# Kernel optimization log

Measured on AMD Instinct MI355X. Metric: run time of the kernel, lower is better.

## Reference

```python
import jax, jax.numpy as jnp
import numpy as np
import math

B, T = 512, 512
ENC = 512          # 2 * input_size
N_MELS, R = 80, 2
ATTN, DEC = 256, 256
PRE_H, PRE_O = 256, 256
HID = 128          # DCA hidden
SC, SK = 8, 21     # static channels / kernel
DC, DK = 8, 21     # dynamic channels / kernel
PL, PA, PB = 11, 0.1, 0.9  # prior length, alpha, beta


def _betabinom_pmf(k, n, a, b):
    lg = math.lgamma
    return math.exp(lg(n + 1) - lg(k + 1) - lg(n - k + 1)
                    + lg(k + a) + lg(n - k + b) - lg(n + a + b)
                    - (lg(a) + lg(b) - lg(a + b)))


def setup_inputs() -> dict:
    key = jax.random.key(0)
    ks = iter(jax.random.split(key, 64))
    def rn(shape, s=0.05):
        return jax.random.normal(next(ks), shape, dtype=jnp.float32) * s
    inp = {}
    inp["h"] = rn([B, T, ENC], 1.0)
    inp["y"] = rn([B, N_MELS], 1.0)
    a = jax.random.uniform(next(ks), [B, T], dtype=jnp.float32)
    inp["alpha"] = a / a.sum(-1, keepdims=True)  # valid attention distribution
    inp["c"] = rn([B, ENC], 1.0)
    for n in ["attn_h0", "attn_c0", "rnn1_h0", "rnn1_c0", "rnn2_h0", "rnn2_c0"]:
        inp[n] = rn([B, ATTN], 1.0)
    # prenet
    inp["fc1_w"] = rn([PRE_H, N_MELS]); inp["fc1_b"] = rn([PRE_H])
    inp["fc2_w"] = rn([PRE_O, PRE_H]); inp["fc2_b"] = rn([PRE_O])
    # dynamic convolution attention
    inp["W_w"] = rn([HID, ATTN]); inp["W_b"] = rn([HID])
    inp["V_w"] = rn([DC * DK, HID])
    inp["F_w"] = rn([SC, 1, SK])
    inp["U_w"] = rn([HID, SC])
    inp["T_w"] = rn([HID, DC]); inp["T_b"] = rn([HID])
    inp["v_w"] = rn([1, HID])
    P = np.array([_betabinom_pmf(k, PL - 1, PA, PB) for k in range(PL)], np.float32)[::-1].copy()
    inp["P"] = jnp.asarray(P)
    # attn LSTM cell: input = 2*input_size + prenet output = 768
    inp["attn_wih"] = rn([4 * ATTN, ENC + PRE_O]); inp["attn_whh"] = rn([4 * ATTN, ATTN])
    inp["attn_bih"] = rn([4 * ATTN]); inp["attn_bhh"] = rn([4 * ATTN])
    inp["lin_w"] = rn([DEC, ENC + ATTN]); inp["lin_b"] = rn([DEC])
    for pfx in ["r1", "r2"]:
        inp[pfx + "_wih"] = rn([4 * DEC, DEC]); inp[pfx + "_whh"] = rn([4 * DEC, DEC])
        inp[pfx + "_bih"] = rn([4 * DEC]); inp[pfx + "_bhh"] = rn([4 * DEC])
    inp["proj_w"] = rn([N_MELS * R, DEC])
    return inp


def _lstm(x, h, c, wih, whh, bih, bhh):
    g = x @ wih.T + bih + h @ whh.T + bhh
    i, f, gg, o = jnp.split(g, 4, axis=-1)
    c2 = jax.nn.sigmoid(f) * c + jax.nn.sigmoid(i) * jnp.tanh(gg)
    return jax.nn.sigmoid(o) * jnp.tanh(c2), c2


def _win(x, k):
    # x: [B, T + k - 1] padded signal -> sliding windows [B, T, k]
    idx = jnp.arange(T)[:, None] + jnp.arange(k)[None, :]
    return x[:, idx]


def reference(h, y, alpha, c, attn_h0, attn_c0, rnn1_h0, rnn1_c0, rnn2_h0, rnn2_c0,
              fc1_w, fc1_b, fc2_w, fc2_b, W_w, W_b, V_w, F_w, U_w, T_w, T_b, v_w, P,
              attn_wih, attn_whh, attn_bih, attn_bhh, lin_w, lin_b,
              r1_wih, r1_whh, r1_bih, r1_bhh, r2_wih, r2_whh, r2_bih, r2_bhh, proj_w):
    # prenet (eval mode -> dropout inactive since fixed=False)
    yp = jax.nn.relu(jax.nn.relu(y @ fc1_w.T + fc1_b) @ fc2_w.T + fc2_b)
    attn_h, attn_c = _lstm(jnp.concatenate([c, yp], -1), attn_h0, attn_c0,
                           attn_wih, attn_whh, attn_bih, attn_bhh)
    # --- dynamic convolution attention ---
    # prior: causal conv with flipped beta-binomial pmf
    p = jnp.einsum('btk,k->bt', _win(jnp.pad(alpha, ((0, 0), (PL - 1, 0))), PL), P)
    p = jnp.log(jnp.clip(p, 1e-6))
    # dynamic filters per batch element: [B, DC, DK]
    G = (jnp.tanh(attn_h @ W_w.T + W_b) @ V_w.T).reshape(-1, DC, DK)
    wd = _win(jnp.pad(alpha, ((0, 0), ((DK - 1) // 2, (DK - 1) // 2))), DK)  # [B,T,DK]
    g = jnp.einsum('btk,bck->btc', wd, G)  # grouped conv1d, groups=B
    ws = _win(jnp.pad(alpha, ((0, 0), ((SK - 1) // 2, (SK - 1) // 2))), SK)
    f = jnp.einsum('btk,ck->btc', ws, F_w[:, 0, :])  # static conv1d
    e = jnp.squeeze(jnp.tanh(f @ U_w.T + g @ T_w.T + T_b) @ v_w.T, -1) + p
    alpha2 = jax.nn.softmax(e, axis=-1)
    # --- context + decoder stack ---
    c2 = jnp.einsum('bt,btd->bd', alpha2, h)
    x = jnp.concatenate([c2, attn_h], -1) @ lin_w.T + lin_b
    r1_h, r1_c = _lstm(x, rnn1_h0, rnn1_c0, r1_wih, r1_whh, r1_bih, r1_bhh)
    x = x + r1_h
    r2_h, r2_c = _lstm(x, rnn2_h0, rnn2_c0, r2_wih, r2_whh, r2_bih, r2_bhh)
    x = x + r2_h
    out = (x @ proj_w.T).reshape(-1, N_MELS, R)
    return (out, alpha2, c2, attn_h, attn_c, r1_h, r1_c, r2_h, r2_c)
```

## Files before the change

### kernel.cpp

```cpp
#include <hip/hip_runtime.h>

typedef unsigned short u16;
typedef __attribute__((ext_vector_type(8))) short s8v;
typedef __attribute__((ext_vector_type(4))) float f32x4;

__device__ __forceinline__ float bf2f(u16 u) { return __uint_as_float(((unsigned)u) << 16); }
__device__ __forceinline__ u16 f2bf(float f) {
    unsigned u = __float_as_uint(f);
    return (u16)((u + 0x7fffu + ((u >> 16) & 1u)) >> 16);
}
__device__ __forceinline__ float ldraw(const void* p, size_t i, int dt) {
    return dt ? ((const float*)p)[i] : bf2f(((const u16*)p)[i]);
}
__device__ __forceinline__ int fl(const int* F, int f) { return f < 0 ? 1 : F[f]; }
__device__ __forceinline__ float fast_tanh(float x) {
    x = fminf(fmaxf(x, -15.f), 15.f);
    float e = __expf(2.f * x);
    return (e - 1.f) / (e + 1.f);
}
__device__ __forceinline__ float sigm(float x) { return 1.f / (1.f + __expf(-x)); }

__global__ __launch_bounds__(256) void k_detect(int* __restrict__ flagsRaw,
    const void* p0, const void* p1, const void* p2, const void* p3, const void* p4,
    const void* p5, const void* p6, const void* p7, const void* p8, const void* p9,
    const void* p10, const void* p11, const void* p12, const void* p13, const void* p14,
    const void* p15, const void* p16, const void* p17, const void* p18, const void* p19,
    const void* p20, const void* p21, const void* p22, const void* p23, const void* p24,
    const void* p25, const void* p26, const void* p27, const void* p28, const void* p29,
    const void* p30, const void* p31, const void* p32, const void* p33, const void* p34,
    const void* p35, const void* p36, const void* p37)
{
    const void* ptrs[38] = {p0,p1,p2,p3,p4,p5,p6,p7,p8,p9,p10,p11,p12,p13,p14,p15,p16,
                            p17,p18,p19,p20,p21,p22,p23,p24,p25,p26,p27,p28,p29,p30,p31,
                            p32,p33,p34,p35,p36,p37};
    const int ns[38] = {134217728, 40960, 262144, 262144,
                        131072,131072,131072,131072,131072,131072,
                        20480,256,65536,256,
                        32768,128,21504,168,1024,1024,128,128,11,
                        786432,262144,1024,1024, 196608,256,
                        262144,262144,1024,1024, 262144,262144,1024,1024, 40960};
    __shared__ int s;
    int b = blockIdx.x, tid = threadIdx.x;
    if (tid == 0) s = 0;
    __syncthreads();
    int nsamp = ns[b] >> 1;
    if (nsamp > 512) nsamp = 512;
    const u16* q = (const u16*)ptrs[b];
    int bad = 0;
    for (int i = tid; i < nsamp; i += 256) {
        u16 u = q[2 * i];
        int e = (u >> 7) & 0xff;
        bad += (e < 96 || e > 159) ? 1 : 0;
    }
    atomicAdd(&s, bad);
    __syncthreads();
    if (tid == 0) flagsRaw[b] = (s * 4 > nsamp) ? 1 : 0;
}

__global__ __launch_bounds__(256) void k_finish(
    const int* __restrict__ FRAW, int* __restrict__ FF,
    const void* U_w, const void* T_w, const void* T_b, const void* v_w, const void* F_w,
    float* utw, float* tbf, float* vf, float* ff)
{
    __shared__ int sflag[38];
    const int big[38] = {1,1,1,1, 1,1,1,1,1,1, 1,0,1,0,
                         1,0,1,0,1,1,0,0,0, 1,1,1,1, 1,0,
                         1,1,1,1, 1,1,1,1, 1};
    int tid = threadIdx.x;
    if (tid == 0) {
        int s = 0, c = 0;
        for (int i = 0; i < 38; i++) if (big[i]) { s += FRAW[i]; c++; }
        int maj = (s * 2 > c) ? 1 : 0;
        for (int i = 0; i < 38; i++) { int v = big[i] ? FRAW[i] : maj; sflag[i] = v; FF[i] = v; }
    }
    __syncthreads();
    int dU = sflag[18], dT = sflag[19], dTb = sflag[20], dV = sflag[21], dF = sflag[17];
    for (int i = tid; i < 1024; i += 256) {
        int j = i >> 3, c = i & 7;
        utw[j * 16 + c]     = ldraw(U_w, i, dU);
        utw[j * 16 + 8 + c] = ldraw(T_w, i, dT);
    }
    if (tid < 128) { tbf[tid] = ldraw(T_b, tid, dTb); vf[tid] = ldraw(v_w, tid, dV); }
    if (tid < 168) ff[tid] = ldraw(F_w, tid, dF);
}

__device__ __forceinline__ void vg32_pair(const int* F,
    const void* A, int lda, int fa, const void* B, int ldb, int bo, int fb, int K,
    int m0, int n0, int N, int tid, int tx, int ty, float* acc,
    float As[32][68], float Bs[32][68])
{
    int dA = fl(F, fa), dB = fl(F, fb);
    bool fastp = dA && dB;
    for (int k0 = 0; k0 < K; k0 += 64) {
        __syncthreads();
        if (fastp) {
            #pragma unroll
            for (int p = 0; p < 2; p++) {
                int e = tid + p * 256;
                int row = e >> 4, kk = (e & 15) * 4;
                float4 va = {0.f, 0.f, 0.f, 0.f};
                if (k0 + kk < K)
                    va = *(const float4*)((const float*)A + (size_t)(m0 + row) * lda + k0 + kk);
                *(float4*)&As[row][kk] = va;
                int nr = n0 + row;
                float4 vb = {0.f, 0.f, 0.f, 0.f};
                if (nr < N && k0 + kk < K)
                    vb = *(const float4*)((const float*)B + (size_t)nr * ldb + bo + k0 + kk);
                *(float4*)&Bs[row][kk] = vb;
            }
        } else {
            #pragma unroll
            for (int p = 0; p < 8; p++) {
                int e = tid + p * 256;
                int row = e >> 6, kk = e & 63;
                As[row][kk] = (k0 + kk < K) ? ldraw(A, (size_t)(m0 + row) * lda + k0 + kk, dA) : 0.f;
                int nr = n0 + row;
                Bs[row][kk] = (nr < N && k0 + kk < K)
                            ? ldraw(B, (size_t)nr * ldb + bo + k0 + kk, dB) : 0.f;
            }
        }
        __syncthreads();
        #pragma unroll
        for (int kq = 0; kq < 16; kq++) {
            float4 a0 = *(const float4*)&As[ty][kq * 4];
            float4 a1 = *(const float4*)&As[ty + 16][kq * 4];
            float4 b0 = *(const float4*)&Bs[tx][kq * 4];
            float4 b1 = *(const float4*)&Bs[tx + 16][kq * 4];
            acc[0] += a0.x*b0.x + a0.y*b0.y + a0.z*b0.z + a0.w*b0.w;
            acc[1] += a0.x*b1.x + a0.y*b1.y + a0.z*b1.z + a0.w*b1.w;
            acc[2] += a1.x*b0.x + a1.y*b0.y + a1.z*b0.z + a1.w*b0.w;
            acc[3] += a1.x*b1.x + a1.y*b1.y + a1.z*b1.z + a1.w*b1.w;
        }
    }
}

__global__ __launch_bounds__(256) void k_vgemm32(
    const int* __restrict__ F,
    const void* A1, int lda1, int fa1, const void* B1, int ldb1, int bo1, int fb1, int K1,
    const void* A2, int lda2, int fa2, const void* B2, int ldb2, int bo2, int fb2, int K2,
    const void* A3, int lda3, int fa3, const void* B3, int ldb3, int bo3, int fb3, int K3,
    const void* bias1, int fx1, const void* bias2, int fx2,
    float* __restrict__ Cf, int ldc, int N, int act)
{
    __shared__ float As[32][68], Bs[32][68];
    int tid = threadIdx.x, tx = tid & 15, ty = tid >> 4;
    int m0 = blockIdx.y * 32, n0 = blockIdx.x * 32;
    float acc[4] = {0.f, 0.f, 0.f, 0.f};
    vg32_pair(F, A1, lda1, fa1, B1, ldb1, bo1, fb1, K1, m0, n0, N, tid, tx, ty, acc, As, Bs);
    if (A2) vg32_pair(F, A2, lda2, fa2, B2, ldb2, bo2, fb2, K2, m0, n0, N, tid, tx, ty, acc, As, Bs);
    if (A3) vg32_pair(F, A3, lda3, fa3, B3, ldb3, bo3, fb3, K3, m0, n0, N, tid, tx, ty, acc, As, Bs);

    #pragma unroll
    for (int c = 0; c < 2; c++) {
        int n = n0 + tx + c * 16;
        if (n >= N) continue;
        float bias = 0.f;
        if (bias1) bias += ldraw(bias1, n, fl(F, fx1));
        if (bias2) bias += ldraw(bias2, n, fl(F, fx2));
        #pragma unroll
        for (int r = 0; r < 2; r++) {
            float v = acc[r * 2 + c] + bias;
            if (act == 1) v = fmaxf(v, 0.f);
            else if (act == 2) v = fast_tanh(v);
            Cf[(size_t)(m0 + ty + r * 16) * ldc + n] = v;
        }
    }
}

__device__ __forceinline__ void lstm_mfma_piece(const int* F,
    const void* A, int lda, int fa, const void* B, int ldb, int bo, int fb, int K,
    int b0, int j0, int tid, int wave, int lane, f32x4& acc,
    u16 As[16][72], u16 Bs[64][72])
{
    int dA = fl(F, fa), dB = fl(F, fb);
    for (int k0 = 0; k0 < K; k0 += 64) {
        __syncthreads();
        for (int g = tid; g < 640; g += 256) {
            const void* src; int dt; size_t idx; u16* dst;
            if (g < 128) {
                int row = g >> 3, kg = (g & 7) * 8;
                idx = (size_t)(b0 + row) * lda + k0 + kg;
                src = A; dt = dA; dst = &As[row][kg];
            } else {
                int gb = g - 128;
                int row = gb >> 3, kg = (gb & 7) * 8;
                int grow = (row >> 4) * 256 + j0 + (row & 15);
                idx = (size_t)grow * ldb + bo + k0 + kg;
                src = B; dt = dB; dst = &Bs[row][kg];
            }
            if (dt) {
                const float* sp = (const float*)src + idx;
                float4 a = *(const float4*)sp;
                float4 b = *(const float4*)(sp + 4);
                s8v v;
                v[0] = (short)f2bf(a.x); v[1] = (short)f2bf(a.y);
                v[2] = (short)f2bf(a.z); v[3] = (short)f2bf(a.w);
                v[4] = (short)f2bf(b.x); v[5] = (short)f2bf(b.y);
                v[6] = (short)f2bf(b.z); v[7] = (short)f2bf(b.w);
                *(s8v*)dst = v;
            } else {
                *(s8v*)dst = *(const s8v*)((const u16*)src + idx);
            }
        }
        __syncthreads();
        int r = lane & 15, kg = (lane >> 4) * 8;
        s8v a0 = *(const s8v*)&As[r][kg];
        s8v w0 = *(const s8v*)&Bs[wave * 16 + r][kg];
        acc = __builtin_amdgcn_mfma_f32_16x16x32_bf16(a0, w0, acc, 0, 0, 0);
        s8v a1 = *(const s8v*)&As[r][32 + kg];
        s8v w1 = *(const s8v*)&Bs[wave * 16 + r][32 + kg];
        acc = __builtin_amdgcn_mfma_f32_16x16x32_bf16(a1, w1, acc, 0, 0, 0);
    }
}

__global__ __launch_bounds__(256) void k_lstm(
    const int* __restrict__ F,
    const void* A1, int lda1, int fa1, const void* B1, int ldb1, int bo1, int fb1, int K1,
    const void* A2, int lda2, int fa2, const void* B2, int ldb2, int bo2, int fb2, int K2,
    const void* A3, int lda3, int fa3, const void* B3, int ldb3, int bo3, int fb3, int K3,
    const void* bih, int fx1, const void* bhh, int fx2,
    const void* c0, int fc0,
    float* __restrict__ h_out, float* __restrict__ c_out,
    const float* __restrict__ xprev, float* __restrict__ xout)
{
    __shared__ u16 As[16][72];
    __shared__ u16 Bs[64][72];
    __shared__ float sG[4][16][16];
    int tid = threadIdx.x, lane = tid & 63, wave = tid >> 6;
    int j0 = blockIdx.x * 16, b0 = blockIdx.y * 16;
    f32x4 acc = {0.f, 0.f, 0.f, 0.f};
    lstm_mfma_piece(F, A1, lda1, fa1, B1, ldb1, bo1, fb1, K1, b0, j0, tid, wave, lane, acc, As, Bs);
    if (A2) lstm_mfma_piece(F, A2, lda2, fa2, B2, ldb2, bo2, fb2, K2, b0, j0, tid, wave, lane, acc, As, Bs);
    if (A3) lstm_mfma_piece(F, A3, lda3, fa3, B3, ldb3, bo3, fb3, K3, b0, j0, tid, wave, lane, acc, As, Bs);

    #pragma unroll
    for (int r2 = 0; r2 < 4; r2++)
        sG[wave][(lane >> 4) * 4 + r2][lane & 15] = acc[r2];
    __syncthreads();

    int jl = tid & 15, bl = tid >> 4;
    int j = j0 + jl, b = b0 + bl;
    int dx1 = fl(F, fx1), dx2 = fl(F, fx2);
    float gi = sG[0][bl][jl] + ldraw(bih, j, dx1)       + ldraw(bhh, j, dx2);
    float gf = sG[1][bl][jl] + ldraw(bih, j + 256, dx1) + ldraw(bhh, j + 256, dx2);
    float gg = sG[2][bl][jl] + ldraw(bih, j + 512, dx1) + ldraw(bhh, j + 512, dx2);
    float go = sG[3][bl][jl] + ldraw(bih, j + 768, dx1) + ldraw(bhh, j + 768, dx2);
    size_t idx = (size_t)b * 256 + j;
    float cp = ldraw(c0, idx, F[fc0]);
    float cn = sigm(gf) * cp + sigm(gi) * fast_tanh(gg);
    float hn = sigm(go) * fast_tanh(cn);
    h_out[idx] = hn;
    c_out[idx] = cn;
    if (xprev) xout[idx] = xprev[idx] + hn;
}

__global__ __launch_bounds__(256) void k_dca(
    const int* __restrict__ F, const void* __restrict__ alpha, const void* __restrict__ P,
    const float* __restrict__ G, const float* __restrict__ utw, const float* __restrict__ tbf,
    const float* __restrict__ vf, const float* __restrict__ ff,
    float* __restrict__ o_a2)
{
    __shared__ float4 sut[512];
    __shared__ float stb[128], sv[128], sff[168], sgd[168], sal[532], spf[16], sred[8];
    int dA = F[2], dP = F[22];
    int b = blockIdx.x, tid = threadIdx.x;
    for (int i = tid; i < 512; i += 256) sut[i] = ((const float4*)utw)[i];
    if (tid < 128) { stb[tid] = tbf[tid]; sv[tid] = vf[tid]; }
    if (tid < 168) { sff[tid] = ff[tid]; sgd[tid] = G[(size_t)b * 168 + tid]; }
    if (tid < 11)  spf[tid] = ldraw(P, tid, dP);
    for (int i = tid; i < 532; i += 256)
        sal[i] = (i >= 10 && i < 522) ? ldraw(alpha, (size_t)b * 512 + i - 10, dA) : 0.f;
    __syncthreads();

    float e[2];
    #pragma unroll
    for (int q = 0; q < 2; q++) {
        int t = tid + q * 256;
        float aw[21];
        #pragma unroll
        for (int k = 0; k < 21; k++) aw[k] = sal[t + k];
        float pv = 0.f;
        #pragma unroll
        for (int k = 0; k < 11; k++) pv += aw[k] * spf[k];
        float fc[8], gc[8];
        #pragma unroll
        for (int c = 0; c < 8; c++) {
            float s1 = 0.f, s2 = 0.f;
            #pragma unroll
            for (int k = 0; k < 21; k++) {
                s1 += aw[k] * sff[c * 21 + k];
                s2 += aw[k] * sgd[c * 21 + k];
            }
            fc[c] = s1; gc[c] = s2;
        }
        float ev = 0.f;
        #pragma unroll 4
        for (int j = 0; j < 128; j++) {
            float4 u0 = sut[j * 4 + 0], u1 = sut[j * 4 + 1];
            float4 t0 = sut[j * 4 + 2], t1 = sut[j * 4 + 3];
            float a = stb[j];
            a += fc[0] * u0.x + fc[1] * u0.y + fc[2] * u0.z + fc[3] * u0.w;
            a += fc[4] * u1.x + fc[5] * u1.y + fc[6] * u1.z + fc[7] * u1.w;
            a += gc[0] * t0.x + gc[1] * t0.y + gc[2] * t0.z + gc[3] * t0.w;
            a += gc[4] * t1.x + gc[5] * t1.y + gc[6] * t1.z + gc[7] * t1.w;
            ev += fast_tanh(a) * sv[j];
        }
        e[q] = ev + __logf(fmaxf(pv, 1e-6f));
    }

    float m = fmaxf(e[0], e[1]);
    #pragma unroll
    for (int off = 32; off >= 1; off >>= 1) m = fmaxf(m, __shfl_xor(m, off));
    if ((tid & 63) == 0) sred[tid >> 6] = m;
    __syncthreads();
    m = fmaxf(fmaxf(sred[0], sred[1]), fmaxf(sred[2], sred[3]));
    float x0 = __expf(e[0] - m), x1 = __expf(e[1] - m);
    float s = x0 + x1;
    #pragma unroll
    for (int off = 32; off >= 1; off >>= 1) s += __shfl_xor(s, off);
    if ((tid & 63) == 0) sred[4 + (tid >> 6)] = s;
    __syncthreads();
    s = sred[4] + sred[5] + sred[6] + sred[7];
    float inv = 1.f / s;
    o_a2[(size_t)b * 512 + tid]       = x0 * inv;
    o_a2[(size_t)b * 512 + tid + 256] = x1 * inv;
}

__global__ __launch_bounds__(256) void k_c2_part(
    const int* __restrict__ F, const float* __restrict__ a2,
    const void* __restrict__ h, float* __restrict__ part)
{
    int dH = F[0];
    int bi = blockIdx.x;
    int b = bi >> 1, sp = bi & 1;
    int tid = threadIdx.x;
    int dsub = (tid & 63) * 8;
    int tsub = tid >> 6;
    __shared__ float sa[256];
    sa[tid] = a2[(size_t)b * 512 + sp * 256 + tid];
    __syncthreads();
    float acc[8];
    #pragma unroll
    for (int j = 0; j < 8; j++) acc[j] = 0.f;
    size_t rowbase = (size_t)b * 512 + sp * 256;
    if (dH) {
        const float* hf = (const float*)h;
        for (int tt = tsub; tt < 256; tt += 4) {
            float a = sa[tt];
            const float* p = hf + (rowbase + tt) * 512 + dsub;
            float4 v0 = *(const float4*)p, v1 = *(const float4*)(p + 4);
            acc[0] += a * v0.x; acc[1] += a * v0.y; acc[2] += a * v0.z; acc[3] += a * v0.w;
            acc[4] += a * v1.x; acc[5] += a * v1.y; acc[6] += a * v1.z; acc[7] += a * v1.w;
        }
    } else {
        const u16* hb = (const u16*)h;
        for (int tt = tsub; tt < 256; tt += 4) {
            float a = sa[tt];
            const u16* p = hb + (rowbase + tt) * 512 + dsub;
            #pragma unroll
            for (int j = 0; j < 8; j++) acc[j] += a * bf2f(p[j]);
        }
    }
    __shared__ float sacc[256 * 8];
    #pragma unroll
    for (int j = 0; j < 8; j++) sacc[tid * 8 + j] = acc[j];
    __syncthreads();
    if (tid < 64) {
        float* pp = part + ((size_t)sp * 512 + b) * 512 + tid * 8;
        #pragma unroll
        for (int j = 0; j < 8; j++)
            pp[j] = sacc[tid * 8 + j] + sacc[(tid + 64) * 8 + j]
                  + sacc[(tid + 128) * 8 + j] + sacc[(tid + 192) * 8 + j];
    }
}

__global__ void k_c2_red(const float* __restrict__ part, float* __restrict__ o_c2)
{
    int idx = blockIdx.x * 256 + threadIdx.x;
    o_c2[idx] = part[idx] + part[idx + 262144];
}

__global__ void k_plant_direct(float* out0, float v) {
    if (threadIdx.x == 0 && blockIdx.x == 0) out0[0] = v;
}

extern "C" void kernel_launch(void* const* d_in, const int* in_sizes, int n_in,
                              void* d_out, int out_size, void* d_ws, size_t ws_size,
                              hipStream_t stream)
{
    (void)out_size; (void)ws_size;
    float* outf = (float*)d_out;

    static const int exp_sizes[38] = {
        134217728, 40960, 262144, 262144,
        131072,131072,131072,131072,131072,131072,
        20480,256,65536,256,
        32768,128,21504,168,1024,1024,128,128,11,
        786432,262144,1024,1024, 196608,256,
        262144,262144,1024,1024, 262144,262144,1024,1024, 40960};
    int bad = 0;
    if (n_in != 38) bad = 100;
    else for (int i = 0; i < 38; i++)
        if (in_sizes[i] != exp_sizes[i]) { bad = i + 1; break; }
    if (bad) {
        k_plant_direct<<<1, 1, 0, stream>>>(outf, 4194304.f + 65536.f * (float)bad);
        return;
    }

    const void* h_enc  = d_in[0];  const void* y      = d_in[1];
    const void* alpha  = d_in[2];  const void* c_in   = d_in[3];
    const void* ah0    = d_in[4];  const void* ac0    = d_in[5];
    const void* r1h0   = d_in[6];  const void* r1c0   = d_in[7];
    const void* r2h0   = d_in[8];  const void* r2c0   = d_in[9];
    const void* fc1_w  = d_in[10]; const void* fc1_b  = d_in[11];
    const void* fc2_w  = d_in[12]; const void* fc2_b  = d_in[13];
    const void* W_w    = d_in[14]; const void* W_b    = d_in[15];
    const void* V_w    = d_in[16]; const void* F_w    = d_in[17];
    const void* U_w    = d_in[18]; const void* T_w    = d_in[19];
    const void* T_b    = d_in[20]; const void* v_w    = d_in[21];
    const void* P      = d_in[22];
    const void* a_wih  = d_in[23]; const void* a_whh  = d_in[24];
    const void* a_bih  = d_in[25]; const void* a_bhh  = d_in[26];
    const void* lin_w  = d_in[27]; const void* lin_b  = d_in[28];
    const void* r1_wih = d_in[29]; const void* r1_whh = d_in[30];
    const void* r1_bih = d_in[31]; const void* r1_bhh = d_in[32];
    const void* r2_wih = d_in[33]; const void* r2_whh = d_in[34];
    const void* r2_bih = d_in[35]; const void* r2_bhh = d_in[36];
    const void* proj_w = d_in[37];

    char* ws = (char*)d_ws;
    int*   FRAW = (int*)  (ws + 0);
    int*   FF   = (int*)  (ws + 256);
    float* utw  = (float*)(ws + 1024);
    float* tbf  = (float*)(ws + 9216);
    float* vf   = (float*)(ws + 9728);
    float* ffs  = (float*)(ws + 10240);
    float* h1f  = (float*)(ws + 12288);
    float* ypf  = (float*)(ws + 536576);
    float* thf  = (float*)(ws + 1060864);
    float* Gdf  = (float*)(ws + 1323008);
    float* part = (float*)(ws + 1667072);

    float* o_out = outf + 0;
    float* o_a2  = outf + 81920;
    float* o_c2  = outf + 344064;
    float* o_ah  = outf + 606208;
    float* o_ac  = outf + 737280;
    float* o_r1h = outf + 868352;
    float* o_r1c = outf + 999424;
    float* o_r2h = outf + 1130496;
    float* o_r2c = outf + 1261568;

    const void* nv = nullptr;
    dim3 blk(256, 1, 1);

    k_detect<<<38, blk, 0, stream>>>(FRAW,
        d_in[0], d_in[1], d_in[2], d_in[3], d_in[4], d_in[5], d_in[6], d_in[7], d_in[8],
        d_in[9], d_in[10], d_in[11], d_in[12], d_in[13], d_in[14], d_in[15], d_in[16],
        d_in[17], d_in[18], d_in[19], d_in[20], d_in[21], d_in[22], d_in[23], d_in[24],
        d_in[25], d_in[26], d_in[27], d_in[28], d_in[29], d_in[30], d_in[31], d_in[32],
        d_in[33], d_in[34], d_in[35], d_in[36], d_in[37]);
    k_finish<<<1, blk, 0, stream>>>(FRAW, FF, U_w, T_w, T_b, v_w, F_w, utw, tbf, vf, ffs);

    k_vgemm32<<<dim3(8, 16), blk, 0, stream>>>(FF,
        y, 80, 1, fc1_w, 80, 0, 10, 80,
        nv, 0, -1, nv, 0, 0, -1, 0,  nv, 0, -1, nv, 0, 0, -1, 0,
        fc1_b, 11, nv, -1, h1f, 256, 256, 1);
    k_vgemm32<<<dim3(8, 16), blk, 0, stream>>>(FF,
        h1f, 256, -1, fc2_w, 256, 0, 12, 256,
        nv, 0, -1, nv, 0, 0, -1, 0,  nv, 0, -1, nv, 0, 0, -1, 0,
        fc2_b, 13, nv, -1, ypf, 256, 256, 1);

    k_lstm<<<dim3(16, 32), blk, 0, stream>>>(FF,
        c_in, 512, 3, a_wih, 768, 0, 23, 512,
        ypf, 256, -1, a_wih, 768, 512, 23, 256,
        ah0, 256, 4, a_whh, 256, 0, 24, 256,
        a_bih, 25, a_bhh, 26, ac0, 5, o_ah, o_ac, nullptr, nullptr);

    k_vgemm32<<<dim3(4, 16), blk, 0, stream>>>(FF,
        o_ah, 256, -1, W_w, 256, 0, 14, 256,
        nv, 0, -1, nv, 0, 0, -1, 0,  nv, 0, -1, nv, 0, 0, -1, 0,
        W_b, 15, nv, -1, thf, 128, 128, 2);
    k_vgemm32<<<dim3(6, 16), blk, 0, stream>>>(FF,
        thf, 128, -1, V_w, 128, 0, 16, 128,
        nv, 0, -1, nv, 0, 0, -1, 0,  nv, 0, -1, nv, 0, 0, -1, 0,
        nv, -1, nv, -1, Gdf, 168, 168, 0);

    k_dca<<<512, blk, 0, stream>>>(FF, alpha, P, Gdf, utw, tbf, vf, ffs, o_a2);

    k_c2_part<<<1024, blk, 0, stream>>>(FF, o_a2, h_enc, part);
    k_c2_red<<<1024, blk, 0, stream>>>(part, o_c2);

    float* x1f = h1f;
    float* x2f = ypf;
    k_vgemm32<<<dim3(8, 16), blk, 0, stream>>>(FF,
        o_c2, 512, -1, lin_w, 768, 0, 27, 512,
        o_ah, 256, -1, lin_w, 768, 512, 27, 256,
        nv, 0, -1, nv, 0, 0, -1, 0,
        lin_b, 28, nv, -1, x1f, 256, 256, 0);

    k_lstm<<<dim3(16, 32), blk, 0, stream>>>(FF,
        x1f, 256, -1, r1_wih, 256, 0, 29, 256,
        r1h0, 256, 6, r1_whh, 256, 0, 30, 256,
        nv, 0, -1, nv, 0, 0, -1, 0,
        r1_bih, 31, r1_bhh, 32, r1c0, 7, o_r1h, o_r1c, x1f, x2f);

    float* x3f = h1f;
    k_lstm<<<dim3(16, 32), blk, 0, stream>>>(FF,
        x2f, 256, -1, r2_wih, 256, 0, 33, 256,
        r2h0, 256, 8, r2_whh, 256, 0, 34, 256,
        nv, 0, -1, nv, 0, 0, -1, 0,
        r2_bih, 35, r2_bhh, 36, r2c0, 9, o_r2h, o_r2c, x2f, x3f);

    k_vgemm32<<<dim3(5, 16), blk, 0, stream>>>(FF,
        x3f, 256, -1, proj_w, 256, 0, 37, 256,
        nv, 0, -1, nv, 0, 0, -1, 0,  nv, 0, -1, nv, 0, 0, -1, 0,
        nv, -1, nv, -1, o_out, 160, 160, 0);
}
```

Measured before the change: 337.7 us.

## Fuse prenet, DCA filter GEMMs, and c2 reduction into fewer kernels

Merges the two prenet linear layers into one kernel that keeps the hidden activations in shared memory. It does the same for the W/V filter-generation GEMMs, and folds the two-way partial reduction of the context vector into the loading stage of the linear GEMM. This removes three kernel launches and the intermediate global round-trips. In exchange, the fused prenet and filter kernels run on only 16 blocks that loop serially over output tiles, which reduces parallelism. The unused third operand and second bias paths are also removed from the generic GEMM.

Result: slower. 763.2 us (+126.0%).

```diff
diff --git a/kernel.cpp b/kernel.cpp
--- a/kernel.cpp
+++ b/kernel.cpp
@@ -87,7 +87,7 @@
 __device__ __forceinline__ void vg32_pair(const int* F,
     const void* A, int lda, int fa, const void* B, int ldb, int bo, int fb, int K,
     int m0, int n0, int N, int tid, int tx, int ty, float* acc,
-    float As[32][68], float Bs[32][68])
+    float (*As)[68], float (*Bs)[68])
 {
     int dA = fl(F, fa), dB = fl(F, fb);
     bool fastp = dA && dB;
@@ -138,8 +138,7 @@
     const int* __restrict__ F,
     const void* A1, int lda1, int fa1, const void* B1, int ldb1, int bo1, int fb1, int K1,
     const void* A2, int lda2, int fa2, const void* B2, int ldb2, int bo2, int fb2, int K2,
-    const void* A3, int lda3, int fa3, const void* B3, int ldb3, int bo3, int fb3, int K3,
-    const void* bias1, int fx1, const void* bias2, int fx2,
+    const void* bias1, int fx1,
     float* __restrict__ Cf, int ldc, int N, int act)
 {
     __shared__ float As[32][68], Bs[32][68];
@@ -148,7 +147,6 @@
     float acc[4] = {0.f, 0.f, 0.f, 0.f};
     vg32_pair(F, A1, lda1, fa1, B1, ldb1, bo1, fb1, K1, m0, n0, N, tid, tx, ty, acc, As, Bs);
     if (A2) vg32_pair(F, A2, lda2, fa2, B2, ldb2, bo2, fb2, K2, m0, n0, N, tid, tx, ty, acc, As, Bs);
-    if (A3) vg32_pair(F, A3, lda3, fa3, B3, ldb3, bo3, fb3, K3, m0, n0, N, tid, tx, ty, acc, As, Bs);
 
     #pragma unroll
     for (int c = 0; c < 2; c++) {
@@ -156,7 +154,6 @@
         if (n >= N) continue;
         float bias = 0.f;
         if (bias1) bias += ldraw(bias1, n, fl(F, fx1));
-        if (bias2) bias += ldraw(bias2, n, fl(F, fx2));
         #pragma unroll
         for (int r = 0; r < 2; r++) {
             float v = acc[r * 2 + c] + bias;
@@ -167,10 +164,140 @@
     }
 }
 
+__global__ __launch_bounds__(256) void k_pre(
+    const int* __restrict__ F, const void* y, const void* fc1_w, const void* fc1_b,
+    const void* fc2_w, const void* fc2_b, float* __restrict__ ypf)
+{
+    __shared__ float As[32][68], Bs[32][68];
+    __shared__ float sH[32][260];
+    int tid = threadIdx.x, tx = tid & 15, ty = tid >> 4;
+    int m0 = blockIdx.x * 32;
+    int d1b = fl(F, 11), d2b = fl(F, 13);
+    for (int nt = 0; nt < 8; nt++) {
+        float acc[4] = {0.f, 0.f, 0.f, 0.f};
+        vg32_pair(F, y, 80, 1, fc1_w, 80, 0, 10, 80, m0, nt * 32, 256, tid, tx, ty, acc, As, Bs);
+        #pragma unroll
+        for (int c = 0; c < 2; c++) {
+            int n = nt * 32 + tx + c * 16;
+            float bias = ldraw(fc1_b, n, d1b);
+            #pragma unroll
+            for (int r = 0; r < 2; r++)
+                sH[ty + r * 16][n] = fmaxf(acc[r * 2 + c] + bias, 0.f);
+        }
+    }
+    for (int nt = 0; nt < 8; nt++) {
+        float acc[4] = {0.f, 0.f, 0.f, 0.f};
+        vg32_pair(F, (const void*)&sH[0][0], 260, -1, fc2_w, 256, 0, 12, 256,
+                  0, nt * 32, 256, tid, tx, ty, acc, As, Bs);
+        #pragma unroll
+        for (int c = 0; c < 2; c++) {
+            int n = nt * 32 + tx + c * 16;
+            float bias = ldraw(fc2_b, n, d2b);
+            #pragma unroll
+            for (int r = 0; r < 2; r++)
+                ypf[(size_t)(m0 + ty + r * 16) * 256 + n] = fmaxf(acc[r * 2 + c] + bias, 0.f);
+        }
+    }
+}
+
+__global__ __launch_bounds__(256) void k_wv(
+    const int* __restrict__ F, const float* __restrict__ ah,
+    const void* W_w, const void* W_b, const void* V_w, float* __restrict__ Gdf)
+{
+    __shared__ float As[32][68], Bs[32][68];
+    __shared__ float sTh[32][132];
+    int tid = threadIdx.x, tx = tid & 15, ty = tid >> 4;
+    int m0 = blockIdx.x * 32;
+    int dWb = fl(F, 15);
+    for (int nt = 0; nt < 4; nt++) {
+        float acc[4] = {0.f, 0.f, 0.f, 0.f};
+        vg32_pair(F, ah, 256, -1, W_w, 256, 0, 14, 256, m0, nt * 32, 128, tid, tx, ty, acc, As, Bs);
+        #pragma unroll
+        for (int c = 0; c < 2; c++) {
+            int n = nt * 32 + tx + c * 16;
+            float bias = ldraw(W_b, n, dWb);
+            #pragma unroll
+            for (int r = 0; r < 2; r++)
+                sTh[ty + r * 16][n] = fast_tanh(acc[r * 2 + c] + bias);
+        }
+    }
+    for (int nt = 0; nt < 6; nt++) {
+        float acc[4] = {0.f, 0.f, 0.f, 0.f};
+        vg32_pair(F, (const void*)&sTh[0][0], 132, -1, V_w, 128, 0, 16, 128,
+                  0, nt * 32, 168, tid, tx, ty, acc, As, Bs);
+        #pragma unroll
+        for (int c = 0; c < 2; c++) {
+            int n = nt * 32 + tx + c * 16;
+            if (n >= 168) continue;
+            #pragma unroll
+            for (int r = 0; r < 2; r++)
+                Gdf[(size_t)(m0 + ty + r * 16) * 168 + n] = acc[r * 2 + c];
+        }
+    }
+}
+
+__global__ __launch_bounds__(256) void k_lin(
+    const int* __restrict__ F, const float* __restrict__ part, float* __restrict__ o_c2,
+    const float* __restrict__ ah, const void* lin_w, const void* lin_b,
+    float* __restrict__ x1f)
+{
+    __shared__ float As[32][68], Bs[32][68];
+    int tid = threadIdx.x, tx = tid & 15, ty = tid >> 4;
+    int m0 = blockIdx.y * 32, n0 = blockIdx.x * 32;
+    int dB = fl(F, 27);
+    float acc[4] = {0.f, 0.f, 0.f, 0.f};
+    for (int k0 = 0; k0 < 512; k0 += 64) {
+        __syncthreads();
+        #pragma unroll
+        for (int p = 0; p < 2; p++) {
+            int e = tid + p * 256;
+            int row = e >> 4, kk = (e & 15) * 4;
+            size_t idx = (size_t)(m0 + row) * 512 + k0 + kk;
+            float4 va = *(const float4*)(part + idx);
+            float4 vb2 = *(const float4*)(part + idx + 262144);
+            va.x += vb2.x; va.y += vb2.y; va.z += vb2.z; va.w += vb2.w;
+            *(float4*)&As[row][kk] = va;
+            if (blockIdx.x == 0) *(float4*)(o_c2 + idx) = va;
+            int nr = n0 + row;
+            float4 vb;
+            if (dB) {
+                vb = *(const float4*)((const float*)lin_w + (size_t)nr * 768 + k0 + kk);
+            } else {
+                const u16* q = (const u16*)lin_w + (size_t)nr * 768 + k0 + kk;
+                vb.x = bf2f(q[0]); vb.y = bf2f(q[1]); vb.z = bf2f(q[2]); vb.w = bf2f(q[3]);
+            }
+            *(float4*)&Bs[row][kk] = vb;
+        }
+        __syncthreads();
+        #pragma unroll
+        for (int kq = 0; kq < 16; kq++) {
+            float4 a0 = *(const float4*)&As[ty][kq * 4];
+            float4 a1 = *(const float4*)&As[ty + 16][kq * 4];
+            float4 b0 = *(const float4*)&Bs[tx][kq * 4];
+            float4 b1 = *(const float4*)&Bs[tx + 16][kq * 4];
+            acc[0] += a0.x*b0.x + a0.y*b0.y + a0.z*b0.z + a0.w*b0.w;
+            acc[1] += a0.x*b1.x + a0.y*b1.y + a0.z*b1.z + a0.w*b1.w;
+            acc[2] += a1.x*b0.x + a1.y*b0.y + a1.z*b0.z + a1.w*b0.w;
+            acc[3] += a1.x*b1.x + a1.y*b1.y + a1.z*b1.z + a1.w*b1.w;
+        }
+    }
+    vg32_pair(F, ah, 256, -1, lin_w, 768, 512, 27, 256, m0, n0, 256, tid, tx, ty, acc, As, Bs);
+
+    int dbias = fl(F, 28);
+    #pragma unroll
+    for (int c = 0; c < 2; c++) {
+        int n = n0 + tx + c * 16;
+        float bias = ldraw(lin_b, n, dbias);
+        #pragma unroll
+        for (int r = 0; r < 2; r++)
+            x1f[(size_t)(m0 + ty + r * 16) * 256 + n] = acc[r * 2 + c] + bias;
+    }
+}
+
 __device__ __forceinline__ void lstm_mfma_piece(const int* F,
     const void* A, int lda, int fa, const void* B, int ldb, int bo, int fb, int K,
     int b0, int j0, int tid, int wave, int lane, f32x4& acc,
-    u16 As[16][72], u16 Bs[64][72])
+    u16 (*As)[72], u16 (*Bs)[72])
 {
     int dA = fl(F, fa), dB = fl(F, fb);
     for (int k0 = 0; k0 < K; k0 += 64) {
@@ -374,12 +501,6 @@
     }
 }
 
-__global__ void k_c2_red(const float* __restrict__ part, float* __restrict__ o_c2)
-{
-    int idx = blockIdx.x * 256 + threadIdx.x;
-    o_c2[idx] = part[idx] + part[idx + 262144];
-}
-
 __global__ void k_plant_direct(float* out0, float v) {
     if (threadIdx.x == 0 && blockIdx.x == 0) out0[0] = v;
 }
@@ -437,9 +558,8 @@
     float* ffs  = (float*)(ws + 10240);
     float* h1f  = (float*)(ws + 12288);
     float* ypf  = (float*)(ws + 536576);
-    float* thf  = (float*)(ws + 1060864);
-    float* Gdf  = (float*)(ws + 1323008);
-    float* part = (float*)(ws + 1667072);
+    float* Gdf  = (float*)(ws + 1060864);
+    float* part = (float*)(ws + 1404928);
 
     float* o_out = outf + 0;
     float* o_a2  = outf + 81920;
@@ -462,14 +582,7 @@
         d_in[33], d_in[34], d_in[35], d_in[36], d_in[37]);
     k_finish<<<1, blk, 0, stream>>>(FRAW, FF, U_w, T_w, T_b, v_w, F_w, utw, tbf, vf, ffs);
 
-    k_vgemm32<<<dim3(8, 16), blk, 0, stream>>>(FF,
-        y, 80, 1, fc1_w, 80, 0, 10, 80,
-        nv, 0, -1, nv, 0, 0, -1, 0,  nv, 0, -1, nv, 0, 0, -1, 0,
-        fc1_b, 11, nv, -1, h1f, 256, 256, 1);
-    k_vgemm32<<<dim3(8, 16), blk, 0, stream>>>(FF,
-        h1f, 256, -1, fc2_w, 256, 0, 12, 256,
-        nv, 0, -1, nv, 0, 0, -1, 0,  nv, 0, -1, nv, 0, 0, -1, 0,
-        fc2_b, 13, nv, -1, ypf, 256, 256, 1);
+    k_pre<<<16, blk, 0, stream>>>(FF, y, fc1_w, fc1_b, fc2_w, fc2_b, ypf);
 
     k_lstm<<<dim3(16, 32), blk, 0, stream>>>(FF,
         c_in, 512, 3, a_wih, 768, 0, 23, 512,
@@ -477,27 +590,15 @@
         ah0, 256, 4, a_whh, 256, 0, 24, 256,
         a_bih, 25, a_bhh, 26, ac0, 5, o_ah, o_ac, nullptr, nullptr);
 
-    k_vgemm32<<<dim3(4, 16), blk, 0, stream>>>(FF,
-        o_ah, 256, -1, W_w, 256, 0, 14, 256,
-        nv, 0, -1, nv, 0, 0, -1, 0,  nv, 0, -1, nv, 0, 0, -1, 0,
-        W_b, 15, nv, -1, thf, 128, 128, 2);
-    k_vgemm32<<<dim3(6, 16), blk, 0, stream>>>(FF,
-        thf, 128, -1, V_w, 128, 0, 16, 128,
-        nv, 0, -1, nv, 0, 0, -1, 0,  nv, 0, -1, nv, 0, 0, -1, 0,
-        nv, -1, nv, -1, Gdf, 168, 168, 0);
+    k_wv<<<16, blk, 0, stream>>>(FF, o_ah, W_w, W_b, V_w, Gdf);
 
     k_dca<<<512, blk, 0, stream>>>(FF, alpha, P, Gdf, utw, tbf, vf, ffs, o_a2);
 
     k_c2_part<<<1024, blk, 0, stream>>>(FF, o_a2, h_enc, part);
-    k_c2_red<<<1024, blk, 0, stream>>>(part, o_c2);
 
     float* x1f = h1f;
     float* x2f = ypf;
-    k_vgemm32<<<dim3(8, 16), blk, 0, stream>>>(FF,
-        o_c2, 512, -1, lin_w, 768, 0, 27, 512,
-        o_ah, 256, -1, lin_w, 768, 512, 27, 256,
-        nv, 0, -1, nv, 0, 0, -1, 0,
-        lin_b, 28, nv, -1, x1f, 256, 256, 0);
+    k_lin<<<dim3(8, 16), blk, 0, stream>>>(FF, part, o_c2, o_ah, lin_w, lin_b, x1f);
 
     k_lstm<<<dim3(16, 32), blk, 0, stream>>>(FF,
         x1f, 256, -1, r1_wih, 256, 0, 29, 256,
@@ -514,6 +615,6 @@
 
     k_vgemm32<<<dim3(5, 16), blk, 0, stream>>>(FF,
         x3f, 256, -1, proj_w, 256, 0, 37, 256,
-        nv, 0, -1, nv, 0, 0, -1, 0,  nv, 0, -1, nv, 0, 0, -1, 0,
-        nv, -1, nv, -1, o_out, 160, 160, 0);
-}
+        nv, 0, -1, nv, 0, 0, -1, 0,
+        nv, -1, o_out, 160, 160, 0);
+}
```
